# Optimization experiments

Hardware: AMD Instinct MI355X
Metric: run time of the kernel (lower is better)

The kernel has to match this reference:

```python
import jax, jax.numpy as jnp
import numpy as np

N = 100000   # input nodes
M = 100000   # output nodes (size = (N, M))
NNZ = 3_200_000  # edges, avg_degree 32
B = 32       # batch
D = 32       # Kaiming channel dim


def setup_inputs() -> dict:
    key = jax.random.key(0)
    k1, k2, k3 = jax.random.split(key, 3)
    # COO indices: row 0 = src (in [0, N)), row 1 = dst (in [0, M))
    indices = jax.random.randint(k1, (2, NNZ), 0, N, dtype=jnp.int32)
    # Kaiming init: randn * sqrt(2/d), as in the torch module when d is given
    values = jax.random.normal(k2, (NNZ,), dtype=jnp.float32) * np.float32((2.0 / D) ** 0.5)
    bias = jnp.zeros((M, 1), dtype=jnp.float32)
    x = jax.random.normal(k3, (B, N, 1), dtype=jnp.float32)
    return {"x": x, "indices": indices, "values": values, "bias": bias}


def reference(x, indices, values, bias):
    # Equivalent of: for each b, sparse.mm(W.T, x[b]) + bias, W in COO (N, M)
    # y[b, m] = sum_{e: dst[e]==m} values[e] * x[b, src[e]] + bias[m]
    src = indices[0]
    dst = indices[1]
    contrib = x[:, src, 0] * values[None, :]           # (B, NNZ) gather-multiply
    y = jax.ops.segment_sum(contrib.T, dst, num_segments=M)  # (M, B) scatter-add
    return (y.T + bias[:, 0][None, :])[..., None]       # (B, M, 1)
```

## Files before the change

### kernel.cpp

```cpp
#include <hip/hip_runtime.h>
#include <hip/hip_fp16.h>
#include <stdint.h>

#define NB 32
#define CSHIFT 7
#define CROWS 128
#define NC_MAX 1024
#define FCHUNK 8192
#define FTHREADS 512
#define EPT (FCHUNK / FTHREADS)
#define HSTAGE 4096
#define CAP_C 4608
#define GTHREADS 512
#define NGW 8
#define GEPT ((CAP_C + GTHREADS - 1) / GTHREADS)
#define HCAP 2816
#define SRC_BITS 18
#define SRC_MASK ((1u << SRC_BITS) - 1)


__global__ void transpose_x_kernel(const float* __restrict__ x,
                                   __half* __restrict__ xt,
                                   int* __restrict__ zeroRegion, int N) {
    __shared__ float tile[32][33];
    if (blockIdx.x == 0) {
        int i = threadIdx.y * 32 + threadIdx.x;
        for (; i < NC_MAX + 4; i += 256) zeroRegion[i] = 0;
    }
    int n0 = blockIdx.x * 32;
    for (int i = threadIdx.y; i < 32; i += 8) {
        int n = n0 + threadIdx.x;
        tile[i][threadIdx.x] = (n < N) ? x[(size_t)i * N + n] : 0.f;
    }
    __syncthreads();
    for (int i = threadIdx.y; i < 32; i += 8) {
        int n = n0 + i;
        if (n < N) xt[(size_t)n * NB + threadIdx.x] =
            __float2half(tile[threadIdx.x][i]);
    }
}

__global__ __launch_bounds__(FTHREADS) void fill_coarse(
        const int* __restrict__ src,
        const int* __restrict__ dst,
        const float* __restrict__ vals,
        int* __restrict__ cCursor,
        uint2* __restrict__ csr,
        int* __restrict__ ovCount,
        int* __restrict__ ovList,
        int nnz) {
    __shared__ uint2 stage[HSTAGE];
    __shared__ unsigned short sbin[HSTAGE];
    __shared__ int lhist[NC_MAX];
    __shared__ int lbase[NC_MAX];
    __shared__ int delta[NC_MAX];
    int t = threadIdx.x;
    int e0 = blockIdx.x * FCHUNK;
    int chunk = min(FCHUNK, nnz - e0);
    int      bcache[EPT];
    uint32_t mcache[EPT];
    uint32_t vcache[EPT];
    int      pcache[EPT];
    for (int i = t; i < NC_MAX; i += FTHREADS) lhist[i] = 0;
    __syncthreads();
#pragma unroll
    for (int q = 0; q < EPT; ++q) {
        int e = e0 + q * FTHREADS + t;
        if (e < nnz) {
            int d = dst[e];
            int bin = d >> CSHIFT;
            bcache[q] = bin;
            mcache[q] = ((uint32_t)(d & (CROWS - 1)) << SRC_BITS) |
                        (uint32_t)src[e];
            vcache[q] = __float_as_uint(vals[e]);
            atomicAdd(&lhist[bin], 1);
        } else bcache[q] = -1;
    }
    __syncthreads();
    int s0 = lhist[2 * t];
    int s1 = lhist[2 * t + 1];
    int tsum = s0 + s1;
    lbase[t] = tsum;
    __syncthreads();
    for (int off = 1; off < FTHREADS; off <<= 1) {
        int add = (t >= off) ? lbase[t - off] : 0;
        __syncthreads();
        lbase[t] += add;
        __syncthreads();
    }
    int texcl = lbase[t] - tsum;
    __syncthreads();
    lbase[2 * t]     = texcl;
    lbase[2 * t + 1] = texcl + s0;
    {
        int g0 = s0 ? atomicAdd(&cCursor[2 * t], s0) : 0;
        int g1 = s1 ? atomicAdd(&cCursor[2 * t + 1], s1) : 0;
        delta[2 * t]     = g0 - texcl;
        delta[2 * t + 1] = g1 - (texcl + s0);
        lhist[2 * t]     = 0;
        lhist[2 * t + 1] = 0;
    }
    __syncthreads();
#pragma unroll
    for (int q = 0; q < EPT; ++q) {
        int bin = bcache[q];
        if (bin >= 0) {
            int r = atomicAdd(&lhist[bin], 1);
            int pos = lbase[bin] + r;
            pcache[q] = pos;
            if (delta[bin] + pos >= CAP_C) {
                bcache[q] = -2;
                int op = atomicAdd(ovCount, 1);
                ovList[op] = e0 + q * FTHREADS + t;
            }
        }
    }
    __syncthreads();
    for (int h = 0; h < FCHUNK / HSTAGE; ++h) {
        int lo = h * HSTAGE;
#pragma unroll
        for (int q = 0; q < EPT; ++q) {
            if (bcache[q] != -1) {
                int p = pcache[q];
                if (p >= lo && p < lo + HSTAGE) {
                    int s = p - lo;
                    if (bcache[q] >= 0) {
                        stage[s] = make_uint2(mcache[q], vcache[q]);
                        sbin[s] = (unsigned short)bcache[q];
                    } else sbin[s] = 0xFFFF;
                }
            }
        }
        __syncthreads();
        int lim = min(HSTAGE, chunk - lo);
        for (int idx = t; idx < lim; idx += FTHREADS) {
            unsigned short bo = sbin[idx];
            if (bo != 0xFFFF)
                csr[(size_t)bo * CAP_C + delta[bo] + lo + idx] = stage[idx];
        }
        __syncthreads();
    }
}

__global__ __launch_bounds__(GTHREADS) void region_sort_gather(
        const int* __restrict__ cCursor,
        const uint2* __restrict__ cCsr,
        const __half* __restrict__ xt,
        const float* __restrict__ bias,
        float* __restrict__ out, int M) {
    __shared__ uint2 sorted[HCAP];
    __shared__ int whist[NGW][CROWS];
    __shared__ int rowOff[CROWS];
    __shared__ int rowCnt[CROWS];
    __shared__ int halfBase;
    int c = blockIdx.x;
    int n = min(cCursor[c], CAP_C);
    int t = threadIdx.x;
    int w = t >> 6;
    uint2 ec[GEPT];
    for (int i = t; i < NGW * CROWS; i += GTHREADS) (&whist[0][0])[i] = 0;
    __syncthreads();
    const uint2* reg = cCsr + (size_t)c * CAP_C;
#pragma unroll
    for (int q = 0; q < GEPT; ++q) {
        int j = q * GTHREADS + t;
        if (j < n) {
            uint2 e = reg[j];
            ec[q] = e;
            atomicAdd(&whist[w][(e.x >> SRC_BITS) & (CROWS - 1)], 1);
        }
    }
    __syncthreads();
    int tot = 0;
    if (t < CROWS) {
#pragma unroll
        for (int w2 = 0; w2 < NGW; ++w2) tot += whist[w2][t];
        rowCnt[t] = tot;
        rowOff[t] = tot;
    }
    __syncthreads();
    for (int off = 1; off < CROWS; off <<= 1) {
        int add = (t < CROWS && t >= off) ? rowOff[t - off] : 0;
        __syncthreads();
        if (t < CROWS) rowOff[t] += add;
        __syncthreads();
    }
    if (t < CROWS) {
        int excl = rowOff[t] - rowCnt[t];
        rowOff[t] = excl;
        if (t == 64) halfBase = excl;
        int run = excl;
#pragma unroll
        for (int w2 = 0; w2 < NGW; ++w2) {
            int cn = whist[w2][t];
            whist[w2][t] = run;
            run += cn;
        }
    }
    __syncthreads();
    int g = t >> 5;
    int b = t & 31;
    int half0 = halfBase;
    int half1 = n - halfBase;

    if (half0 <= HCAP && half1 <= HCAP) {
        for (int h = 0; h < 2; ++h) {
            int hb = h ? halfBase : 0;
#pragma unroll
            for (int q = 0; q < GEPT; ++q) {
                int j = q * GTHREADS + t;
                if (j < n) {
                    int row = (ec[q].x >> SRC_BITS) & (CROWS - 1);
                    if ((row >> 6) == h) {
                        int p = atomicAdd(&whist[w][row], 1) - hb;
                        sorted[p] = ec[q];
                    }
                }
            }
            __syncthreads();
            for (int r = (h << 6) + g; r < (h << 6) + 64; r += 16) {
                int m = c * CROWS + r;
                if (m >= M) continue;
                int jj   = rowOff[r] - hb;
                int jend = jj + rowCnt[r];
                float acc0 = 0.f, acc1 = 0.f;
                for (; jj + 8 <= jend; jj += 8) {
                    uint2 e0 = sorted[jj + 0];
                    uint2 e1 = sorted[jj + 1];
                    uint2 e2 = sorted[jj + 2];
                    uint2 e3 = sorted[jj + 3];
                    uint2 e4 = sorted[jj + 4];
                    uint2 e5 = sorted[jj + 5];
                    uint2 e6 = sorted[jj + 6];
                    uint2 e7 = sorted[jj + 7];
                    float x0 = __half2float(xt[(size_t)(e0.x & SRC_MASK) * NB + b]);
                    float x1 = __half2float(xt[(size_t)(e1.x & SRC_MASK) * NB + b]);
                    float x2 = __half2float(xt[(size_t)(e2.x & SRC_MASK) * NB + b]);
                    float x3 = __half2float(xt[(size_t)(e3.x & SRC_MASK) * NB + b]);
                    float x4 = __half2float(xt[(size_t)(e4.x & SRC_MASK) * NB + b]);
                    float x5 = __half2float(xt[(size_t)(e5.x & SRC_MASK) * NB + b]);
                    float x6 = __half2float(xt[(size_t)(e6.x & SRC_MASK) * NB + b]);
                    float x7 = __half2float(xt[(size_t)(e7.x & SRC_MASK) * NB + b]);
                    acc0 = fmaf(__uint_as_float(e0.y), x0, acc0);
                    acc1 = fmaf(__uint_as_float(e1.y), x1, acc1);
                    acc0 = fmaf(__uint_as_float(e2.y), x2, acc0);
                    acc1 = fmaf(__uint_as_float(e3.y), x3, acc1);
                    acc0 = fmaf(__uint_as_float(e4.y), x4, acc0);
                    acc1 = fmaf(__uint_as_float(e5.y), x5, acc1);
                    acc0 = fmaf(__uint_as_float(e6.y), x6, acc0);
                    acc1 = fmaf(__uint_as_float(e7.y), x7, acc1);
                }
                for (; jj < jend; ++jj) {
                    uint2 e = sorted[jj];
                    acc0 = fmaf(__uint_as_float(e.y),
                                __half2float(xt[(size_t)(e.x & SRC_MASK) * NB + b]),
                                acc0);
                }
                out[(size_t)b * M + m] = acc0 + acc1 + bias[m];
            }
            __syncthreads();
        }
    } else {
        for (int r = g; r < CROWS; r += 16) {
            int m = c * CROWS + r;
            if (m >= M) continue;
            float acc = 0.f;
            for (int j = 0; j < n; ++j) {
                uint2 e = reg[j];
                if ((int)((e.x >> SRC_BITS) & (CROWS - 1)) == r)
                    acc = fmaf(__uint_as_float(e.y),
                               __half2float(xt[(size_t)(e.x & SRC_MASK) * NB + b]),
                               acc);
            }
            out[(size_t)b * M + m] = acc + bias[m];
        }
    }
}

__global__ void fixup_kernel(const int* __restrict__ ovCount,
                             const int* __restrict__ ovList,
                             const int* __restrict__ src,
                             const int* __restrict__ dst,
                             const float* __restrict__ vals,
                             const __half* __restrict__ xt,
                             float* __restrict__ out, int M) {
    long long total = (long long)(*ovCount) * 32;
    long long stride = (long long)gridDim.x * blockDim.x;
    for (long long i = (long long)blockIdx.x * blockDim.x + threadIdx.x;
         i < total; i += stride) {
        int k = (int)(i >> 5);
        int b = (int)(i & 31);
        int e = ovList[k];
        atomicAdd(&out[(size_t)b * M + dst[e]],
                  vals[e] * __half2float(xt[(size_t)src[e] * NB + b]));
    }
}

__global__ void finalize_kernel(const float* __restrict__ yt,
                                const float* __restrict__ bias,
                                float* __restrict__ out, int M) {
    __shared__ float tile[32][33];
    int m0 = blockIdx.x * 32;
    for (int i = threadIdx.y; i < 32; i += 8) {
        int m = m0 + i;
        tile[i][threadIdx.x] = (m < M) ? yt[(size_t)m * NB + threadIdx.x] : 0.f;
    }
    __syncthreads();
    for (int i = threadIdx.y; i < 32; i += 8) {
        int m = m0 + threadIdx.x;
        if (m < M) out[(size_t)i * M + m] = tile[threadIdx.x][i] + bias[m];
    }
}

__global__ void scatter_kernel(const int* __restrict__ src,
                               const int* __restrict__ dst,
                               const float* __restrict__ vals,
                               const __half* __restrict__ xt,
                               float* __restrict__ yt, int nnz) {
    long long tid = (long long)blockIdx.x * blockDim.x + threadIdx.x;
    int e = (int)(tid >> 5);
    if (e >= nnz) return;
    int b = (int)(tid & 31);
    atomicAdd(&yt[(size_t)dst[e] * NB + b],
              vals[e] * __half2float(xt[(size_t)src[e] * NB + b]));
}

extern "C" void kernel_launch(void* const* d_in, const int* in_sizes, int n_in,
                              void* d_out, int out_size, void* d_ws, size_t ws_size,
                              hipStream_t stream) {
    const float* x       = (const float*)d_in[0];
    const int*   indices = (const int*)  d_in[1];
    const float* vals    = (const float*)d_in[2];
    const float* bias    = (const float*)d_in[3];

    float* out = (float*)d_out;

    int nnz = in_sizes[1] / 2;
    int N   = in_sizes[0] / NB;
    int M   = in_sizes[3];

    const int* src = indices;
    const int* dst = indices + nnz;

    int ncoarse = (M + CROWS - 1) >> CSHIFT;

    __half* xt      = (__half*)d_ws;
    int*    cCursor = (int*)(xt + (size_t)N * NB);
    int*    ovCount = cCursor + NC_MAX;
    int*    ovList  = ovCount + 4;
    uint2*  cCsr    = (uint2*)(((uintptr_t)(ovList + nnz) + 15) &
                               ~(uintptr_t)15);

    size_t need = (size_t)((char*)(cCsr + (size_t)ncoarse * CAP_C) -
                           (char*)d_ws);

    float* yt = (float*)(xt + (size_t)N * NB);
    size_t need_fb = (size_t)((char*)(yt + (size_t)M * NB) - (char*)d_ws);

    if (ws_size >= need && ncoarse <= NC_MAX) {
        transpose_x_kernel<<<(N + 31) / 32, dim3(32, 8), 0, stream>>>(
            x, xt, cCursor, N);
        int fgrid = (nnz + FCHUNK - 1) / FCHUNK;
        fill_coarse<<<fgrid, FTHREADS, 0, stream>>>(src, dst, vals, cCursor,
                                                    cCsr, ovCount, ovList,
                                                    nnz);
        region_sort_gather<<<ncoarse, GTHREADS, 0, stream>>>(cCursor, cCsr,
                                                             xt, bias, out, M);
        fixup_kernel<<<32, 256, 0, stream>>>(ovCount, ovList, src, dst, vals,
                                             xt, out, M);
    } else if (ws_size >= need_fb) {
        transpose_x_kernel<<<(N + 31) / 32, dim3(32, 8), 0, stream>>>(
            x, xt, cCursor, N);
        hipMemsetAsync(yt, 0, (size_t)M * NB * sizeof(float), stream);
        long long pairs = (long long)nnz * NB;
        int grid = (int)((pairs + 255) / 256);
        scatter_kernel<<<grid, 256, 0, stream>>>(src, dst, vals, xt, yt, nnz);
        finalize_kernel<<<(M + 31) / 32, dim3(32, 8), 0, stream>>>(yt, bias,
                                                                   out, M);
    }
}
```

Baseline: 176.8 us.

## Fuse x transpose into fill kernel and fold overflow fixup into gather

The x transpose moves into extra blocks of the fill kernel, so one launch does both jobs, and a memset now clears the cursors. FCHUNK is halved so each block's whole chunk fits in shared memory, which removes the two-pass staging loop and the pcache array. The separate overflow fixup kernel is removed: each output row scans the overflow list inside region_sort_gather. This saves two kernel launches and their serialization, but a large overflow list would make every row do a linear scan, and the smaller chunks mean more global cursor atomics.

```diff
diff --git a/kernel.cpp b/kernel.cpp
--- a/kernel.cpp
+++ b/kernel.cpp
@@ -6,10 +6,9 @@
 #define CSHIFT 7
 #define CROWS 128
 #define NC_MAX 1024
-#define FCHUNK 8192
+#define FCHUNK 4096
 #define FTHREADS 512
 #define EPT (FCHUNK / FTHREADS)
-#define HSTAGE 4096
 #define CAP_C 4608
 #define GTHREADS 512
 #define NGW 8
@@ -19,28 +18,9 @@
 #define SRC_MASK ((1u << SRC_BITS) - 1)
 
 
-__global__ void transpose_x_kernel(const float* __restrict__ x,
-                                   __half* __restrict__ xt,
-                                   int* __restrict__ zeroRegion, int N) {
-    __shared__ float tile[32][33];
-    if (blockIdx.x == 0) {
-        int i = threadIdx.y * 32 + threadIdx.x;
-        for (; i < NC_MAX + 4; i += 256) zeroRegion[i] = 0;
-    }
-    int n0 = blockIdx.x * 32;
-    for (int i = threadIdx.y; i < 32; i += 8) {
-        int n = n0 + threadIdx.x;
-        tile[i][threadIdx.x] = (n < N) ? x[(size_t)i * N + n] : 0.f;
-    }
-    __syncthreads();
-    for (int i = threadIdx.y; i < 32; i += 8) {
-        int n = n0 + i;
-        if (n < N) xt[(size_t)n * NB + threadIdx.x] =
-            __float2half(tile[threadIdx.x][i]);
-    }
-}
-
-__global__ __launch_bounds__(FTHREADS) void fill_coarse(
+__global__ __launch_bounds__(FTHREADS) void fill_and_transpose(
+        const float* __restrict__ x,
+        __half* __restrict__ xt, int N,
         const int* __restrict__ src,
         const int* __restrict__ dst,
         const float* __restrict__ vals,
@@ -48,19 +28,37 @@
         uint2* __restrict__ csr,
         int* __restrict__ ovCount,
         int* __restrict__ ovList,
-        int nnz) {
-    __shared__ uint2 stage[HSTAGE];
-    __shared__ unsigned short sbin[HSTAGE];
+        int nnz, int fblocks) {
+    __shared__ uint2 stage[FCHUNK];
+    __shared__ unsigned short sbin[FCHUNK];
     __shared__ int lhist[NC_MAX];
     __shared__ int lbase[NC_MAX];
     __shared__ int delta[NC_MAX];
     int t = threadIdx.x;
+
+    if (blockIdx.x >= fblocks) {
+        float* tile = (float*)stage;
+        int blk = blockIdx.x - fblocks;
+        int tx = t & 31, ty = t >> 5;
+        int n0 = blk * 32;
+        for (int i = ty; i < 32; i += 16) {
+            int n = n0 + tx;
+            tile[i * 33 + tx] = (n < N) ? x[(size_t)i * N + n] : 0.f;
+        }
+        __syncthreads();
+        for (int i = ty; i < 32; i += 16) {
+            int n = n0 + i;
+            if (n < N) xt[(size_t)n * NB + tx] =
+                __float2half(tile[tx * 33 + i]);
+        }
+        return;
+    }
+
     int e0 = blockIdx.x * FCHUNK;
     int chunk = min(FCHUNK, nnz - e0);
     int      bcache[EPT];
     uint32_t mcache[EPT];
     uint32_t vcache[EPT];
-    int      pcache[EPT];
     for (int i = t; i < NC_MAX; i += FTHREADS) lhist[i] = 0;
     __syncthreads();
 #pragma unroll
@@ -107,38 +105,21 @@
         if (bin >= 0) {
             int r = atomicAdd(&lhist[bin], 1);
             int pos = lbase[bin] + r;
-            pcache[q] = pos;
-            if (delta[bin] + pos >= CAP_C) {
-                bcache[q] = -2;
+            if (delta[bin] + pos < CAP_C) {
+                stage[pos] = make_uint2(mcache[q], vcache[q]);
+                sbin[pos] = (unsigned short)bin;
+            } else {
+                sbin[pos] = 0xFFFF;
                 int op = atomicAdd(ovCount, 1);
                 ovList[op] = e0 + q * FTHREADS + t;
             }
         }
     }
     __syncthreads();
-    for (int h = 0; h < FCHUNK / HSTAGE; ++h) {
-        int lo = h * HSTAGE;
-#pragma unroll
-        for (int q = 0; q < EPT; ++q) {
-            if (bcache[q] != -1) {
-                int p = pcache[q];
-                if (p >= lo && p < lo + HSTAGE) {
-                    int s = p - lo;
-                    if (bcache[q] >= 0) {
-                        stage[s] = make_uint2(mcache[q], vcache[q]);
-                        sbin[s] = (unsigned short)bcache[q];
-                    } else sbin[s] = 0xFFFF;
-                }
-            }
-        }
-        __syncthreads();
-        int lim = min(HSTAGE, chunk - lo);
-        for (int idx = t; idx < lim; idx += FTHREADS) {
-            unsigned short bo = sbin[idx];
-            if (bo != 0xFFFF)
-                csr[(size_t)bo * CAP_C + delta[bo] + lo + idx] = stage[idx];
-        }
-        __syncthreads();
+    for (int idx = t; idx < chunk; idx += FTHREADS) {
+        unsigned short bo = sbin[idx];
+        if (bo != 0xFFFF)
+            csr[(size_t)bo * CAP_C + delta[bo] + idx] = stage[idx];
     }
 }
 
@@ -147,6 +128,11 @@
         const uint2* __restrict__ cCsr,
         const __half* __restrict__ xt,
         const float* __restrict__ bias,
+        const int* __restrict__ ovCount,
+        const int* __restrict__ ovList,
+        const int* __restrict__ src,
+        const int* __restrict__ dst,
+        const float* __restrict__ vals,
         float* __restrict__ out, int M) {
     __shared__ uint2 sorted[HCAP];
     __shared__ int whist[NGW][CROWS];
@@ -157,6 +143,7 @@
     int n = min(cCursor[c], CAP_C);
     int t = threadIdx.x;
     int w = t >> 6;
+    int ovN = *ovCount;
     uint2 ec[GEPT];
     for (int i = t; i < NGW * CROWS; i += GTHREADS) (&whist[0][0])[i] = 0;
     __syncthreads();
@@ -256,6 +243,15 @@
                                 __half2float(xt[(size_t)(e.x & SRC_MASK) * NB + b]),
                                 acc0);
                 }
+                if (ovN) {
+                    for (int k = 0; k < ovN; ++k) {
+                        int e = ovList[k];
+                        if (dst[e] == m)
+                            acc0 = fmaf(vals[e],
+                                __half2float(xt[(size_t)src[e] * NB + b]),
+                                acc0);
+                    }
+                }
                 out[(size_t)b * M + m] = acc0 + acc1 + bias[m];
             }
             __syncthreads();
@@ -272,43 +268,32 @@
                                __half2float(xt[(size_t)(e.x & SRC_MASK) * NB + b]),
                                acc);
             }
+            if (ovN) {
+                for (int k = 0; k < ovN; ++k) {
+                    int e = ovList[k];
+                    if (dst[e] == m)
+                        acc = fmaf(vals[e],
+                            __half2float(xt[(size_t)src[e] * NB + b]), acc);
+                }
+            }
             out[(size_t)b * M + m] = acc + bias[m];
         }
     }
 }
 
-__global__ void fixup_kernel(const int* __restrict__ ovCount,
-                             const int* __restrict__ ovList,
-                             const int* __restrict__ src,
-                             const int* __restrict__ dst,
-                             const float* __restrict__ vals,
-                             const __half* __restrict__ xt,
-                             float* __restrict__ out, int M) {
-    long long total = (long long)(*ovCount) * 32;
-    long long stride = (long long)gridDim.x * blockDim.x;
-    for (long long i = (long long)blockIdx.x * blockDim.x + threadIdx.x;
-         i < total; i += stride) {
-        int k = (int)(i >> 5);
-        int b = (int)(i & 31);
-        int e = ovList[k];
-        atomicAdd(&out[(size_t)b * M + dst[e]],
-                  vals[e] * __half2float(xt[(size_t)src[e] * NB + b]));
-    }
-}
-
-__global__ void finalize_kernel(const float* __restrict__ yt,
-                                const float* __restrict__ bias,
-                                float* __restrict__ out, int M) {
+__global__ void transpose_x_kernel(const float* __restrict__ x,
+                                   __half* __restrict__ xt, int N) {
     __shared__ float tile[32][33];
-    int m0 = blockIdx.x * 32;
+    int n0 = blockIdx.x * 32;
     for (int i = threadIdx.y; i < 32; i += 8) {
-        int m = m0 + i;
-        tile[i][threadIdx.x] = (m < M) ? yt[(size_t)m * NB + threadIdx.x] : 0.f;
+        int n = n0 + threadIdx.x;
+        tile[i][threadIdx.x] = (n < N) ? x[(size_t)i * N + n] : 0.f;
     }
     __syncthreads();
     for (int i = threadIdx.y; i < 32; i += 8) {
-        int m = m0 + threadIdx.x;
-        if (m < M) out[(size_t)i * M + m] = tile[threadIdx.x][i] + bias[m];
+        int n = n0 + i;
+        if (n < N) xt[(size_t)n * NB + threadIdx.x] =
+            __float2half(tile[threadIdx.x][i]);
     }
 }
 
@@ -325,6 +310,22 @@
               vals[e] * __half2float(xt[(size_t)src[e] * NB + b]));
 }
 
+__global__ void finalize_kernel(const float* __restrict__ yt,
+                                const float* __restrict__ bias,
+                                float* __restrict__ out, int M) {
+    __shared__ float tile[32][33];
+    int m0 = blockIdx.x * 32;
+    for (int i = threadIdx.y; i < 32; i += 8) {
+        int m = m0 + i;
+        tile[i][threadIdx.x] = (m < M) ? yt[(size_t)m * NB + threadIdx.x] : 0.f;
+    }
+    __syncthreads();
+    for (int i = threadIdx.y; i < 32; i += 8) {
+        int m = m0 + threadIdx.x;
+        if (m < M) out[(size_t)i * M + m] = tile[threadIdx.x][i] + bias[m];
+    }
+}
+
 extern "C" void kernel_launch(void* const* d_in, const int* in_sizes, int n_in,
                               void* d_out, int out_size, void* d_ws, size_t ws_size,
                               hipStream_t stream) {
@@ -358,19 +359,16 @@
     size_t need_fb = (size_t)((char*)(yt + (size_t)M * NB) - (char*)d_ws);
 
     if (ws_size >= need && ncoarse <= NC_MAX) {
-        transpose_x_kernel<<<(N + 31) / 32, dim3(32, 8), 0, stream>>>(
-            x, xt, cCursor, N);
-        int fgrid = (nnz + FCHUNK - 1) / FCHUNK;
-        fill_coarse<<<fgrid, FTHREADS, 0, stream>>>(src, dst, vals, cCursor,
-                                                    cCsr, ovCount, ovList,
-                                                    nnz);
-        region_sort_gather<<<ncoarse, GTHREADS, 0, stream>>>(cCursor, cCsr,
-                                                             xt, bias, out, M);
-        fixup_kernel<<<32, 256, 0, stream>>>(ovCount, ovList, src, dst, vals,
-                                             xt, out, M);
+        hipMemsetAsync(cCursor, 0, (NC_MAX + 4) * sizeof(int), stream);
+        int fblocks = (nnz + FCHUNK - 1) / FCHUNK;
+        int tblocks = (N + 31) / 32;
+        fill_and_transpose<<<fblocks + tblocks, FTHREADS, 0, stream>>>(
+            x, xt, N, src, dst, vals, cCursor, cCsr, ovCount, ovList,
+            nnz, fblocks);
+        region_sort_gather<<<ncoarse, GTHREADS, 0, stream>>>(
+            cCursor, cCsr, xt, bias, ovCount, ovList, src, dst, vals, out, M);
     } else if (ws_size >= need_fb) {
-        transpose_x_kernel<<<(N + 31) / 32, dim3(32, 8), 0, stream>>>(
-            x, xt, cCursor, N);
+        transpose_x_kernel<<<(N + 31) / 32, dim3(32, 8), 0, stream>>>(x, xt, N);
         hipMemsetAsync(yt, 0, (size_t)M * NB * sizeof(float), stream);
         long long pairs = (long long)nnz * NB;
         int grid = (int)((pairs + 255) / 256);
```

Measured after the change: 191.9 us. +8.6%, slower.
